# Kernel tuning notes

Hardware: AMD Instinct MI355X
Metric: run time of the kernel (lower is better)

Reference implementation:

```python
import jax, jax.numpy as jnp
import numpy as np

IN_DIM, HIDDEN_DIM, LATENT_DIM = 512, 1024, 256
B, N = 64, 1024


def setup_inputs() -> dict:
    key = jax.random.key(0)
    ks = jax.random.split(key, 8)
    x = jax.random.normal(ks[0], (B, N, IN_DIM), dtype=jnp.float32)
    a = jax.random.uniform(ks[1], (B, N, N), dtype=jnp.float32)
    s1 = 1.0 / np.sqrt(IN_DIM)
    s2 = 1.0 / np.sqrt(HIDDEN_DIM)
    W1 = jax.random.uniform(ks[2], (HIDDEN_DIM, IN_DIM), jnp.float32, -s1, s1)
    b1 = jax.random.uniform(ks[3], (HIDDEN_DIM,), jnp.float32, -s1, s1)
    W_mu = jax.random.uniform(ks[4], (LATENT_DIM, HIDDEN_DIM), jnp.float32, -s2, s2)
    b_mu = jax.random.uniform(ks[5], (LATENT_DIM,), jnp.float32, -s2, s2)
    W_lv = jax.random.uniform(ks[6], (LATENT_DIM, HIDDEN_DIM), jnp.float32, -s2, s2)
    b_lv = jax.random.uniform(ks[7], (LATENT_DIM,), jnp.float32, -s2, s2)
    return {"x": x, "a": a, "W1": W1, "b1": b1, "W_mu": W_mu, "b_mu": b_mu,
            "W_lv": W_lv, "b_lv": b_lv}


def normalize_adj(a):
    # A_hat = A + I; D^{-1/2} A_hat D^{-1/2} expressed as row/col scaling
    n = a.shape[-1]
    a_hat = a + jnp.eye(n, dtype=a.dtype)
    deg = a_hat.sum(axis=-1)                      # [B, N]
    d = (deg + 1e-8) ** -0.5                      # [B, N]
    return a_hat * d[..., :, None] * d[..., None, :]


def reference(x, a, W1, b1, W_mu, b_mu, W_lv, b_lv):
    a_norm = normalize_adj(a)                     # [B, N, N]
    h = jnp.einsum('bnm,bmd->bnd', a_norm, x)     # message passing
    h = jax.nn.relu(jnp.einsum('bnd,hd->bnh', h, W1) + b1)
    mu = jnp.einsum('bnh,lh->bnl', h, W_mu) + b_mu
    logvar = jnp.einsum('bnh,lh->bnl', h, W_lv) + b_lv
    return (mu, logvar)
```

## Files before the change

kernel.cpp:

```cpp
#include <hip/hip_runtime.h>
#include <hip/hip_bf16.h>

typedef unsigned short u16;
typedef __attribute__((ext_vector_type(8))) short s16x8;
typedef __attribute__((ext_vector_type(4))) float f32x4;

__device__ __forceinline__ u16 f2bf(float f) {
    union { float f; unsigned u; } c; c.f = f;
    unsigned r = c.u + 0x7fffu + ((c.u >> 16) & 1u);
    return (u16)(r >> 16);
}

__device__ __forceinline__ void gld_lds16(const u16* g, u16* l) {
    __builtin_amdgcn_global_load_lds(
        (const __attribute__((address_space(1))) void*)g,
        (__attribute__((address_space(3))) void*)l, 16, 0, 0);
}

template<bool CVT>
__global__ __launch_bounds__(256) void rowsum_kernel(const float* __restrict__ a,
                                                     float* __restrict__ dsc,
                                                     u16* __restrict__ ab) {
    const int wave = threadIdx.x >> 6, lane = threadIdx.x & 63;
    const long row = (long)blockIdx.x * 4 + wave;
    const int diag = (int)(row & 1023);
    const float4* a4 = (const float4*)(a + row * 1024);
    float s = 0.f;
    #pragma unroll
    for (int i = 0; i < 4; ++i) {
        float4 v = a4[i * 64 + lane];
        s += v.x + v.y + v.z + v.w;
        if (CVT) {
            const int c0 = (i * 64 + lane) * 4;
            float e[4] = {v.x, v.y, v.z, v.w};
            if (diag >= c0 && diag < c0 + 4) e[diag - c0] += 1.0f;
            union { u16 u[4]; uint2 w; } cv;
            cv.u[0] = f2bf(e[0]); cv.u[1] = f2bf(e[1]);
            cv.u[2] = f2bf(e[2]); cv.u[3] = f2bf(e[3]);
            *(uint2*)(ab + row * 1024 + c0) = cv.w;
        }
    }
    #pragma unroll
    for (int off = 32; off > 0; off >>= 1) s += __shfl_down(s, off, 64);
    if (lane == 0) dsc[row] = rsqrtf(s + 1.0f + 1e-8f);
}

__global__ __launch_bounds__(256) void xst_kernel(const float* __restrict__ x,
                                                  const float* __restrict__ dsc,
                                                  u16* __restrict__ xst) {
    __shared__ u16 ls[64][65];
    const int b  = blockIdx.z;
    const int n0 = blockIdx.x * 64;
    const int j0 = blockIdx.y * 64;
    const int t  = threadIdx.x;
    {
        int jj = t >> 4, nn = (t & 15) * 4;
        #pragma unroll
        for (int it = 0; it < 4; ++it, jj += 16) {
            float dj = dsc[b * 1024 + j0 + jj];
            float4 v = *(const float4*)(x + ((long)(b * 1024 + j0 + jj)) * 512 + n0 + nn);
            ls[jj][nn + 0] = f2bf(v.x * dj);
            ls[jj][nn + 1] = f2bf(v.y * dj);
            ls[jj][nn + 2] = f2bf(v.z * dj);
            ls[jj][nn + 3] = f2bf(v.w * dj);
        }
    }
    __syncthreads();
    {
        int nn = t >> 2;
        int jv = (t & 3) * 8;
        #pragma unroll
        for (int it = 0; it < 2; ++it, jv += 32) {
            union { u16 u[8]; uint4 w; } cv;
            #pragma unroll
            for (int u = 0; u < 8; ++u) cv.u[u] = ls[jv + u][nn];
            *(uint4*)(xst + ((long)b * 512 + n0 + nn) * 1024 + j0 + jv) = cv.w;
        }
    }
}

__global__ __launch_bounds__(256) void cvt_weights(const float* __restrict__ W1,
                                                   const float* __restrict__ Wmu,
                                                   const float* __restrict__ Wlv,
                                                   u16* __restrict__ w1b,
                                                   u16* __restrict__ wml) {
    int i = blockIdx.x * 256 + threadIdx.x;
    w1b[i] = f2bf(W1[i]);
    wml[i] = f2bf(i < 262144 ? Wmu[i] : Wlv[i - 262144]);
}

template<int EPI>
__global__ __launch_bounds__(512, 2) void gemm256(
    const u16* __restrict__ A, const u16* __restrict__ Bt,
    int K, long aBStride, long bBStride,
    const float* __restrict__ dsc,
    u16* __restrict__ outb,
    const float* __restrict__ bias0, const float* __restrict__ bias1,
    float* __restrict__ outMu, float* __restrict__ outLv)
{
    __shared__ __align__(16) u16 As[2][256 * 32];
    __shared__ __align__(16) u16 Bs[2][256 * 32];

    const int gx = gridDim.x, gy = gridDim.y;
    const int nwg = gx * gy * gridDim.z;
    const int fid = (blockIdx.z * gy + blockIdx.y) * gx + blockIdx.x;
    int swz = fid;
    if (!(nwg & 7)) swz = (fid & 7) * (nwg >> 3) + (fid >> 3);
    const int bx  = swz % gx;
    const int tmp = swz / gx;
    const int by  = tmp % gy;
    const int bz  = tmp / gy;

    const u16* Ab = A + (long)bz * aBStride;
    const u16* Bb = Bt + (long)bz * bBStride;
    const int n0 = bx * 256, m0 = by * 256;
    const int T = (int)threadIdx.x;
    const int wid = T >> 6, lane = T & 63, quad = lane >> 4, tr = lane & 15;
    const int wm = (wid >> 2) * 128;
    const int wn = (wid & 3) * 64;
    const int NT = K >> 5;

    const int sr   = T >> 2;
    const int scol = ((T & 3) ^ (sr & 3)) << 3;
    const u16* gA = Ab + (long)(m0 + sr) * K + scol;
    const u16* gB = Bb + (long)(n0 + sr) * K + scol;
    const long rowK = (long)128 * K;
    u16* const wA0 = &As[0][0] + wid * 512;
    u16* const wB0 = &Bs[0][0] + wid * 512;
    u16* const wA1 = &As[1][0] + wid * 512;
    u16* const wB1 = &Bs[1][0] + wid * 512;

    f32x4 acc[8][4];
    #pragma unroll
    for (int i = 0; i < 8; ++i)
        #pragma unroll
        for (int j = 0; j < 4; ++j) acc[i][j] = (f32x4){0.f, 0.f, 0.f, 0.f};

    gld_lds16(gA,           wA0); gld_lds16(gA + rowK,        wA0 + 4096);
    gld_lds16(gB,           wB0); gld_lds16(gB + rowK,        wB0 + 4096);
    gld_lds16(gA + 32,      wA1); gld_lds16(gA + 32 + rowK,   wA1 + 4096);
    gld_lds16(gB + 32,      wB1); gld_lds16(gB + 32 + rowK,   wB1 + 4096);
    asm volatile("s_waitcnt vmcnt(4)" ::: "memory");
    __builtin_amdgcn_s_barrier();
    __builtin_amdgcn_sched_barrier(0);

    const u16* rdA  = &As[0][0]; const u16* rdB  = &Bs[0][0];
    const u16* rdA2 = &As[1][0]; const u16* rdB2 = &Bs[1][0];
    u16* stA = wA0; u16* stB = wB0;
    u16* stA2 = wA1; u16* stB2 = wB1;

    const int rofs = (quad ^ (tr & 3)) << 3;
    const int rbA  = (wm + tr) * 32 + rofs;

    for (int t = 0; t < NT; ++t) {
        s16x8 af[4], bfv[4];
        #pragma unroll
        for (int i = 0; i < 4; ++i) af[i]  = *(const s16x8*)&rdA[rbA + i * 512];
        #pragma unroll
        for (int i = 0; i < 4; ++i) bfv[i] = *(const s16x8*)&rdB[(wn + i * 16 + tr) * 32 + rofs];
        __builtin_amdgcn_s_barrier();
        asm volatile("s_waitcnt lgkmcnt(0)" ::: "memory");
        __builtin_amdgcn_sched_barrier(0);
        __builtin_amdgcn_s_setprio(1);
        #pragma unroll
        for (int mi = 0; mi < 4; ++mi)
            #pragma unroll
            for (int ni = 0; ni < 4; ++ni)
                acc[mi][ni] = __builtin_amdgcn_mfma_f32_16x16x32_bf16(af[mi], bfv[ni], acc[mi][ni], 0, 0, 0);
        __builtin_amdgcn_s_setprio(0);
        __builtin_amdgcn_s_barrier();
        #pragma unroll
        for (int i = 0; i < 4; ++i) af[i] = *(const s16x8*)&rdA[rbA + 2048 + i * 512];
        __builtin_amdgcn_s_barrier();
        asm volatile("s_waitcnt lgkmcnt(0)" ::: "memory");
        __builtin_amdgcn_sched_barrier(0);
        __builtin_amdgcn_s_setprio(1);
        #pragma unroll
        for (int mi = 0; mi < 4; ++mi)
            #pragma unroll
            for (int ni = 0; ni < 4; ++ni)
                acc[mi + 4][ni] = __builtin_amdgcn_mfma_f32_16x16x32_bf16(af[mi], bfv[ni], acc[mi + 4][ni], 0, 0, 0);
        __builtin_amdgcn_s_setprio(0);
        __builtin_amdgcn_s_barrier();
        __builtin_amdgcn_sched_barrier(0);
        if (t + 2 < NT) {
            const u16* a = gA + (long)(t + 2) * 32;
            const u16* b = gB + (long)(t + 2) * 32;
            gld_lds16(a, stA); gld_lds16(a + rowK, stA + 4096);
            gld_lds16(b, stB); gld_lds16(b + rowK, stB + 4096);
            asm volatile("s_waitcnt vmcnt(4)" ::: "memory");
        } else if (t + 1 < NT) {
            asm volatile("s_waitcnt vmcnt(0)" ::: "memory");
        }
        __builtin_amdgcn_s_barrier();
        __builtin_amdgcn_sched_barrier(0);
        const u16* tA = rdA; rdA = rdA2; rdA2 = tA;
        const u16* tB = rdB; rdB = rdB2; rdB2 = tB;
        u16* sA = stA; stA = stA2; stA2 = sA;
        u16* sB = stB; stB = stB2; stB2 = sB;
    }

    if constexpr (EPI == 1) {
        #pragma unroll
        for (int mi = 0; mi < 8; ++mi) {
            const int gmB = m0 + wm + mi * 16 + quad * 4;
            #pragma unroll
            for (int r = 0; r < 4; ++r) {
                const long row = (long)bz * 1024 + gmB + r;
                const float d = dsc[row];
                #pragma unroll
                for (int ni = 0; ni < 4; ++ni) {
                    const int gn = n0 + wn + ni * 16 + tr;
                    outb[row * 512 + gn] = f2bf(d * acc[mi][ni][r]);
                }
            }
        }
    } else if constexpr (EPI == 2) {
        float bb[4];
        #pragma unroll
        for (int ni = 0; ni < 4; ++ni) bb[ni] = bias0[n0 + wn + ni * 16 + tr];
        #pragma unroll
        for (int mi = 0; mi < 8; ++mi) {
            const long gmB = m0 + wm + mi * 16 + quad * 4;
            #pragma unroll
            for (int ni = 0; ni < 4; ++ni) {
                const int gn = n0 + wn + ni * 16 + tr;
                #pragma unroll
                for (int r = 0; r < 4; ++r) {
                    float hv = acc[mi][ni][r] + bb[ni];
                    outb[(gmB + r) * 1024 + gn] = f2bf(hv > 0.f ? hv : 0.f);
                }
            }
        }
    } else {
        float* op       = (n0 == 0) ? outMu : outLv;
        const float* bp = (n0 == 0) ? bias0 : bias1;
        float bb[4];
        #pragma unroll
        for (int ni = 0; ni < 4; ++ni) bb[ni] = bp[wn + ni * 16 + tr];
        #pragma unroll
        for (int mi = 0; mi < 8; ++mi) {
            const long gmB = m0 + wm + mi * 16 + quad * 4;
            #pragma unroll
            for (int ni = 0; ni < 4; ++ni) {
                const int cn = wn + ni * 16 + tr;
                #pragma unroll
                for (int r = 0; r < 4; ++r)
                    op[(gmB + r) * 256 + cn] = acc[mi][ni][r] + bb[ni];
            }
        }
    }
}

__global__ __launch_bounds__(256) void gemm_f32a(
    const float* __restrict__ A, const u16* __restrict__ Bt,
    const float* __restrict__ dsc, const float* __restrict__ xin,
    u16* __restrict__ outb)
{
    __shared__ __align__(16) u16 As[128 * 40];
    __shared__ __align__(16) u16 Bs[128 * 40];
    const int bz = blockIdx.z;
    const float* Ab = A + (long)bz * 1024 * 1024;
    const u16* Bb = Bt + (long)bz * 512 * 1024;
    const int n0 = blockIdx.x * 128, m0 = blockIdx.y * 128;
    const int t = threadIdx.x;
    const int wave = t >> 6, lane = t & 63, quad = lane >> 4, tr = lane & 15;
    const int wm = (wave >> 1) * 64, wn = (wave & 1) * 64;
    const int K = 1024;

    f32x4 acc[4][4];
    #pragma unroll
    for (int i = 0; i < 4; ++i)
        #pragma unroll
        for (int j = 0; j < 4; ++j) acc[i][j] = (f32x4){0.f, 0.f, 0.f, 0.f};

    const int mm = t >> 2, kk = (t & 3) * 8;
    for (int k0 = 0; k0 < K; k0 += 32) {
        #pragma unroll
        for (int it = 0; it < 2; ++it) {
            const int r = mm + it * 64;
            const float4* p = (const float4*)(Ab + (long)(m0 + r) * K + k0 + kk);
            float4 v0 = p[0], v1 = p[1];
            union { u16 u[8]; uint4 w; } cv;
            cv.u[0]=f2bf(v0.x); cv.u[1]=f2bf(v0.y); cv.u[2]=f2bf(v0.z); cv.u[3]=f2bf(v0.w);
            cv.u[4]=f2bf(v1.x); cv.u[5]=f2bf(v1.y); cv.u[6]=f2bf(v1.z); cv.u[7]=f2bf(v1.w);
            *(uint4*)&As[r * 40 + kk] = cv.w;
            uint4 v = *(const uint4*)(Bb + (long)(n0 + r) * K + k0 + kk);
            *(uint4*)&Bs[r * 40 + kk] = v;
        }
        __syncthreads();
        s16x8 af[4], bfv[4];
        #pragma unroll
        for (int mi = 0; mi < 4; ++mi)
            af[mi] = *(const s16x8*)&As[(wm + mi * 16 + tr) * 40 + quad * 8];
        #pragma unroll
        for (int ni = 0; ni < 4; ++ni)
            bfv[ni] = *(const s16x8*)&Bs[(wn + ni * 16 + tr) * 40 + quad * 8];
        #pragma unroll
        for (int mi = 0; mi < 4; ++mi)
            #pragma unroll
            for (int ni = 0; ni < 4; ++ni)
                acc[mi][ni] = __builtin_amdgcn_mfma_f32_16x16x32_bf16(af[mi], bfv[ni], acc[mi][ni], 0, 0, 0);
        __syncthreads();
    }
    #pragma unroll
    for (int mi = 0; mi < 4; ++mi)
        #pragma unroll
        for (int ni = 0; ni < 4; ++ni) {
            const int gn = n0 + wn + ni * 16 + tr;
            #pragma unroll
            for (int r = 0; r < 4; ++r) {
                const int gm = m0 + wm + mi * 16 + quad * 4 + r;
                long row = (long)bz * 1024 + gm;
                float di = dsc[row];
                outb[row * 512 + gn] = f2bf(di * (acc[mi][ni][r] + di * xin[row * 512 + gn]));
            }
        }
}

extern "C" void kernel_launch(void* const* d_in, const int* in_sizes, int n_in,
                              void* d_out, int out_size, void* d_ws, size_t ws_size,
                              hipStream_t stream) {
    const float* x   = (const float*)d_in[0];
    const float* a   = (const float*)d_in[1];
    const float* W1  = (const float*)d_in[2];
    const float* b1  = (const float*)d_in[3];
    const float* Wmu = (const float*)d_in[4];
    const float* bmu = (const float*)d_in[5];
    const float* Wlv = (const float*)d_in[6];
    const float* blv = (const float*)d_in[7];
    float* out = (float*)d_out;

    char* base = (char*)d_ws;
    size_t off = 0;
    auto take = [&](size_t bytes) { char* p = base + off; off += (bytes + 255) & ~(size_t)255; return p; };
    float* dsc = (float*)take((size_t)65536 * 4);
    u16*  xst  = (u16*)take((size_t)64 * 512 * 1024 * 2);
    u16*  h    = (u16*)take((size_t)65536 * 512 * 2);
    u16*  hid  = (u16*)take((size_t)65536 * 1024 * 2);
    u16*  w1b  = (u16*)take((size_t)1024 * 512 * 2);
    u16*  wml  = (u16*)take((size_t)512 * 1024 * 2);
    u16*  ab   = (u16*)take((size_t)64 * 1024 * 1024 * 2);
    const bool useAb = (off <= ws_size);

    if (useAb) rowsum_kernel<true ><<<16384, 256, 0, stream>>>(a, dsc, ab);
    else       rowsum_kernel<false><<<16384, 256, 0, stream>>>(a, dsc, nullptr);
    xst_kernel<<<dim3(8, 16, 64), 256, 0, stream>>>(x, dsc, xst);
    cvt_weights<<<2048, 256, 0, stream>>>(W1, Wmu, Wlv, w1b, wml);

    if (useAb)
        gemm256<1><<<dim3(2, 4, 64), 512, 0, stream>>>(
            ab, xst, 1024, 1024L * 1024, 512L * 1024,
            dsc, h, nullptr, nullptr, nullptr, nullptr);
    else
        gemm_f32a<<<dim3(4, 8, 64), 256, 0, stream>>>(a, xst, dsc, x, h);

    gemm256<2><<<dim3(4, 256, 1), 512, 0, stream>>>(
        h, w1b, 512, 0, 0, nullptr, hid, b1, nullptr, nullptr, nullptr);

    gemm256<3><<<dim3(2, 256, 1), 512, 0, stream>>>(
        hid, wml, 1024, 0, 0, nullptr, nullptr, bmu, blv,
        out, out + (size_t)65536 * 256);
}
```

Baseline: 841.2 us.

## Deepen bf16 GEMM LDS pipeline to four stages with dynamic shared memory

The shared GEMM kernel moves from a double-buffered LDS ring to a 4-slot ring in 128 KB of dynamic shared memory, keeping three global-to-LDS tile loads in flight. The second A-fragment read and the next stage's global loads are now issued before the second MFMA batch, and the explicit lgkmcnt waits are dropped. The LDS XOR swizzle now uses bits 1-2 of the row instead of bits 0-1 to cut bank conflicts. The 128 KB LDS footprint likely limits the kernel to one 512-thread workgroup per CU instead of two, trading occupancy for deeper prefetch.

```diff
diff --git a/kernel.cpp b/kernel.cpp
--- a/kernel.cpp
+++ b/kernel.cpp
@@ -98,8 +98,9 @@
     const float* __restrict__ bias0, const float* __restrict__ bias1,
     float* __restrict__ outMu, float* __restrict__ outLv)
 {
-    __shared__ __align__(16) u16 As[2][256 * 32];
-    __shared__ __align__(16) u16 Bs[2][256 * 32];
+    extern __shared__ __align__(16) u16 smem[];
+    u16* const Asl = smem;
+    u16* const Bsl = smem + 4 * 8192;
 
     const int gx = gridDim.x, gy = gridDim.y;
     const int nwg = gx * gy * gridDim.z;
@@ -121,14 +122,11 @@
     const int NT = K >> 5;
 
     const int sr   = T >> 2;
-    const int scol = ((T & 3) ^ (sr & 3)) << 3;
+    const int scol = ((T & 3) ^ ((sr >> 1) & 3)) << 3;
     const u16* gA = Ab + (long)(m0 + sr) * K + scol;
     const u16* gB = Bb + (long)(n0 + sr) * K + scol;
     const long rowK = (long)128 * K;
-    u16* const wA0 = &As[0][0] + wid * 512;
-    u16* const wB0 = &Bs[0][0] + wid * 512;
-    u16* const wA1 = &As[1][0] + wid * 512;
-    u16* const wB1 = &Bs[1][0] + wid * 512;
+    const int wofs = wid * 512;
 
     f32x4 acc[8][4];
     #pragma unroll
@@ -136,69 +134,66 @@
         #pragma unroll
         for (int j = 0; j < 4; ++j) acc[i][j] = (f32x4){0.f, 0.f, 0.f, 0.f};
 
-    gld_lds16(gA,           wA0); gld_lds16(gA + rowK,        wA0 + 4096);
-    gld_lds16(gB,           wB0); gld_lds16(gB + rowK,        wB0 + 4096);
-    gld_lds16(gA + 32,      wA1); gld_lds16(gA + 32 + rowK,   wA1 + 4096);
-    gld_lds16(gB + 32,      wB1); gld_lds16(gB + 32 + rowK,   wB1 + 4096);
-    asm volatile("s_waitcnt vmcnt(4)" ::: "memory");
+    const int rofs = (quad ^ ((tr >> 1) & 3)) << 3;
+    const int rbA  = (wm + tr) * 32 + rofs;
+    const int rbB  = (wn + tr) * 32 + rofs;
+
+    #define STAGE(slot, t) do {                                         \
+        const u16* ga_ = gA + (long)(t) * 32;                           \
+        const u16* gb_ = gB + (long)(t) * 32;                           \
+        u16* la_ = Asl + (slot) * 8192 + wofs;                          \
+        u16* lb_ = Bsl + (slot) * 8192 + wofs;                          \
+        gld_lds16(ga_, la_); gld_lds16(ga_ + rowK, la_ + 4096);         \
+        gld_lds16(gb_, lb_); gld_lds16(gb_ + rowK, lb_ + 4096);         \
+    } while (0)
+
+    STAGE(0, 0); STAGE(1, 1); STAGE(2, 2);
+    asm volatile("s_waitcnt vmcnt(8)" ::: "memory");
     __builtin_amdgcn_s_barrier();
     __builtin_amdgcn_sched_barrier(0);
 
-    const u16* rdA  = &As[0][0]; const u16* rdB  = &Bs[0][0];
-    const u16* rdA2 = &As[1][0]; const u16* rdB2 = &Bs[1][0];
-    u16* stA = wA0; u16* stB = wB0;
-    u16* stA2 = wA1; u16* stB2 = wB1;
-
-    const int rofs = (quad ^ (tr & 3)) << 3;
-    const int rbA  = (wm + tr) * 32 + rofs;
-
     for (int t = 0; t < NT; ++t) {
-        s16x8 af[4], bfv[4];
-        #pragma unroll
-        for (int i = 0; i < 4; ++i) af[i]  = *(const s16x8*)&rdA[rbA + i * 512];
-        #pragma unroll
-        for (int i = 0; i < 4; ++i) bfv[i] = *(const s16x8*)&rdB[(wn + i * 16 + tr) * 32 + rofs];
+        const u16* rdA = Asl + (t & 3) * 8192;
+        const u16* rdB = Bsl + (t & 3) * 8192;
+        s16x8 af0[4], bfv[4], af1[4];
+        #pragma unroll
+        for (int i = 0; i < 4; ++i) af0[i] = *(const s16x8*)&rdA[rbA + i * 512];
+        #pragma unroll
+        for (int i = 0; i < 4; ++i) bfv[i] = *(const s16x8*)&rdB[rbB + i * 512];
         __builtin_amdgcn_s_barrier();
-        asm volatile("s_waitcnt lgkmcnt(0)" ::: "memory");
         __builtin_amdgcn_sched_barrier(0);
         __builtin_amdgcn_s_setprio(1);
         #pragma unroll
         for (int mi = 0; mi < 4; ++mi)
             #pragma unroll
             for (int ni = 0; ni < 4; ++ni)
-                acc[mi][ni] = __builtin_amdgcn_mfma_f32_16x16x32_bf16(af[mi], bfv[ni], acc[mi][ni], 0, 0, 0);
-        __builtin_amdgcn_s_setprio(0);
-        __builtin_amdgcn_s_barrier();
-        #pragma unroll
-        for (int i = 0; i < 4; ++i) af[i] = *(const s16x8*)&rdA[rbA + 2048 + i * 512];
-        __builtin_amdgcn_s_barrier();
-        asm volatile("s_waitcnt lgkmcnt(0)" ::: "memory");
-        __builtin_amdgcn_sched_barrier(0);
-        __builtin_amdgcn_s_setprio(1);
-        #pragma unroll
-        for (int mi = 0; mi < 4; ++mi)
-            #pragma unroll
-            for (int ni = 0; ni < 4; ++ni)
-                acc[mi + 4][ni] = __builtin_amdgcn_mfma_f32_16x16x32_bf16(af[mi], bfv[ni], acc[mi + 4][ni], 0, 0, 0);
+                acc[mi][ni] = __builtin_amdgcn_mfma_f32_16x16x32_bf16(af0[mi], bfv[ni], acc[mi][ni], 0, 0, 0);
         __builtin_amdgcn_s_setprio(0);
         __builtin_amdgcn_s_barrier();
         __builtin_amdgcn_sched_barrier(0);
-        if (t + 2 < NT) {
-            const u16* a = gA + (long)(t + 2) * 32;
-            const u16* b = gB + (long)(t + 2) * 32;
-            gld_lds16(a, stA); gld_lds16(a + rowK, stA + 4096);
-            gld_lds16(b, stB); gld_lds16(b + rowK, stB + 4096);
+        #pragma unroll
+        for (int i = 0; i < 4; ++i) af1[i] = *(const s16x8*)&rdA[rbA + 2048 + i * 512];
+        if (t + 3 < NT) {
+            STAGE((t + 3) & 3, t + 3);
+            asm volatile("s_waitcnt vmcnt(8)" ::: "memory");
+        } else if (t + 2 < NT) {
             asm volatile("s_waitcnt vmcnt(4)" ::: "memory");
         } else if (t + 1 < NT) {
             asm volatile("s_waitcnt vmcnt(0)" ::: "memory");
         }
         __builtin_amdgcn_s_barrier();
         __builtin_amdgcn_sched_barrier(0);
-        const u16* tA = rdA; rdA = rdA2; rdA2 = tA;
-        const u16* tB = rdB; rdB = rdB2; rdB2 = tB;
-        u16* sA = stA; stA = stA2; stA2 = sA;
-        u16* sB = stB; stB = stB2; stB2 = sB;
-    }
+        __builtin_amdgcn_s_setprio(1);
+        #pragma unroll
+        for (int mi = 0; mi < 4; ++mi)
+            #pragma unroll
+            for (int ni = 0; ni < 4; ++ni)
+                acc[mi + 4][ni] = __builtin_amdgcn_mfma_f32_16x16x32_bf16(af1[mi], bfv[ni], acc[mi + 4][ni], 0, 0, 0);
+        __builtin_amdgcn_s_setprio(0);
+        __builtin_amdgcn_s_barrier();
+        __builtin_amdgcn_sched_barrier(0);
+    }
+    #undef STAGE
 
     if constexpr (EPI == 1) {
         #pragma unroll
@@ -331,6 +326,14 @@
     const float* blv = (const float*)d_in[7];
     float* out = (float*)d_out;
 
+    static bool attrDone = false;
+    if (!attrDone) {
+        (void)hipFuncSetAttribute((const void*)gemm256<1>, hipFuncAttributeMaxDynamicSharedMemorySize, 131072);
+        (void)hipFuncSetAttribute((const void*)gemm256<2>, hipFuncAttributeMaxDynamicSharedMemorySize, 131072);
+        (void)hipFuncSetAttribute((const void*)gemm256<3>, hipFuncAttributeMaxDynamicSharedMemorySize, 131072);
+        attrDone = true;
+    }
+
     char* base = (char*)d_ws;
     size_t off = 0;
     auto take = [&](size_t bytes) { char* p = base + off; off += (bytes + 255) & ~(size_t)255; return p; };
@@ -349,16 +352,16 @@
     cvt_weights<<<2048, 256, 0, stream>>>(W1, Wmu, Wlv, w1b, wml);
 
     if (useAb)
-        gemm256<1><<<dim3(2, 4, 64), 512, 0, stream>>>(
+        gemm256<1><<<dim3(2, 4, 64), 512, 131072, stream>>>(
             ab, xst, 1024, 1024L * 1024, 512L * 1024,
             dsc, h, nullptr, nullptr, nullptr, nullptr);
     else
         gemm_f32a<<<dim3(4, 8, 64), 256, 0, stream>>>(a, xst, dsc, x, h);
 
-    gemm256<2><<<dim3(4, 256, 1), 512, 0, stream>>>(
+    gemm256<2><<<dim3(4, 256, 1), 512, 131072, stream>>>(
         h, w1b, 512, 0, 0, nullptr, hid, b1, nullptr, nullptr, nullptr);
 
-    gemm256<3><<<dim3(2, 256, 1), 512, 0, stream>>>(
+    gemm256<3><<<dim3(2, 256, 1), 512, 131072, stream>>>(
         hid, wml, 1024, 0, 0, nullptr, nullptr, bmu, blv,
         out, out + (size_t)65536 * 256);
 }
```

New measurement: 768.1 us. 8.7% less time.
